# Optimization experiments

Measured on AMD Instinct MI355X. Metric: run time of the kernel, lower is better.

The kernel has to match this reference:

```python
import jax, jax.numpy as jnp
import numpy as np

D_MODEL = 1024
N_HEADS = 16
D_HEAD = D_MODEL // N_HEADS
B = 2
Q_LEN = 1024
MEM_LEN = 1024
K_LEN = MEM_LEN + Q_LEN


def _split_heads(x, n_heads):
    b, t, d = x.shape
    return x.reshape(b, t, n_heads, d // n_heads).transpose(0, 2, 1, 3)


def _rel_shift(x):
    # x: [b, h, q, k] -> Transformer-XL relative shift
    b, h, q_len, k_len = x.shape
    x = jnp.pad(x, ((0, 0), (0, 0), (0, 0), (1, 0)))
    x = x.reshape(b, h, k_len + 1, q_len)
    x = x[:, :, 1:, :]
    return x.reshape(b, h, q_len, k_len)


def setup_inputs() -> dict:
    key = jax.random.key(0)
    ks = jax.random.split(key, 10)
    s = 1.0 / np.sqrt(D_MODEL)  # lecun_normal-ish scale for kernels
    return {
        "h": jax.random.normal(ks[0], (B, Q_LEN, D_MODEL), jnp.float32),
        "mem": jax.random.normal(ks[1], (B, MEM_LEN, D_MODEL), jnp.float32),
        "r": jax.random.normal(ks[2], (K_LEN, D_MODEL), jnp.float32),
        "Wq": jax.random.normal(ks[3], (D_MODEL, D_MODEL), jnp.float32) * s,
        "Wk": jax.random.normal(ks[4], (D_MODEL, D_MODEL), jnp.float32) * s,
        "Wv": jax.random.normal(ks[5], (D_MODEL, D_MODEL), jnp.float32) * s,
        "Wr": jax.random.normal(ks[6], (D_MODEL, D_MODEL), jnp.float32) * s,
        "Wo": jax.random.normal(ks[7], (D_MODEL, D_MODEL), jnp.float32) * s,
        "r_w_bias": jnp.zeros((N_HEADS, D_HEAD), jnp.float32),
        "r_r_bias": jnp.zeros((N_HEADS, D_HEAD), jnp.float32),
    }


def reference(h, mem, r, Wq, Wk, Wv, Wr, Wo, r_w_bias, r_r_bias):
    k_len = mem.shape[1] + h.shape[1]
    cat = jnp.concatenate([mem, h], axis=1)           # [b, k, d]
    q = _split_heads(h @ Wq, N_HEADS)                  # [b, h, q, dh]
    k = _split_heads(cat @ Wk, N_HEADS)                # [b, h, k, dh]
    v = _split_heads(cat @ Wv, N_HEADS)                # [b, h, k, dh]
    r_head = (r @ Wr).reshape(k_len, N_HEADS, D_HEAD).transpose(1, 0, 2)  # [h, k, dh]

    qw = q + r_w_bias[None, :, None, :]
    ac = jnp.einsum('bhqd,bhkd->bhqk', qw, k)          # content score
    qr = q + r_r_bias[None, :, None, :]
    bd = _rel_shift(jnp.einsum('bhqd,hkd->bhqk', qr, r_head))  # position score

    attn_score = (ac + bd) / jnp.sqrt(jnp.array(D_HEAD, jnp.float32))
    attn_prob = jax.nn.softmax(attn_score, axis=-1)
    attn_vec = jnp.einsum('bhqk,bhkd->bhqd', attn_prob, v)
    b, nh, t, dh = attn_vec.shape
    attn_vec = attn_vec.transpose(0, 2, 1, 3).reshape(b, t, nh * dh)
    return attn_vec @ Wo
```

## Files before the change

kernel.cpp:

```cpp
#include <hip/hip_runtime.h>

#define DM 1024
#define NH 16
#define DH 64
#define QL 1024
#define KL 2048

typedef short s16x8 __attribute__((ext_vector_type(8)));
typedef float f32x4 __attribute__((ext_vector_type(4)));

__device__ __forceinline__ unsigned short f2bf(float f) {
  unsigned int u = __builtin_bit_cast(unsigned int, f);
  u += 0x7fffu + ((u >> 16) & 1u);
  return (unsigned short)(u >> 16);
}
__device__ __forceinline__ float bf2f(unsigned short b) {
  unsigned int u = ((unsigned int)b) << 16;
  return __builtin_bit_cast(float, u);
}
__device__ __forceinline__ f32x4 mfma16(s16x8 a, s16x8 b, f32x4 c) {
  return __builtin_amdgcn_mfma_f32_16x16x32_bf16(a, b, c, 0, 0, 0);
}
__device__ __forceinline__ void gl2lds16(const void* g, void* l) {
  __builtin_amdgcn_global_load_lds(
      (const __attribute__((address_space(1))) unsigned int*)g,
      (__attribute__((address_space(3))) unsigned int*)l, 16, 0, 0);
}


__global__ __launch_bounds__(256) void prep_all(
    const float* __restrict__ h, const float* __restrict__ mem, const float* __restrict__ r,
    const float* __restrict__ Wq, const float* __restrict__ Wk, const float* __restrict__ Wv,
    const float* __restrict__ Wr, const float* __restrict__ Wo,
    unsigned short* __restrict__ catb, unsigned short* __restrict__ rb,
    unsigned short* __restrict__ wqt, unsigned short* __restrict__ wkvt,
    unsigned short* __restrict__ wrt,
    unsigned short* __restrict__ wohi, unsigned short* __restrict__ wolo)
{
  __shared__ unsigned short tH[64][72];
  __shared__ unsigned short tL[64][72];
  if (blockIdx.x < 6144) {
    int idx = blockIdx.x * 256 + threadIdx.x;
    if (idx < 1048576) {
      int e = idx * 4;
      int row = e >> 10, col = e & 1023;
      int b = row >> 11, t = row & 2047;
      const float* s = (t < 1024) ? &mem[((size_t)(b * 1024 + t)) * 1024 + col]
                                  : &h[((size_t)(b * 1024 + t - 1024)) * 1024 + col];
      float4 v = *(const float4*)s;
      *(ushort4*)&catb[e] = make_ushort4(f2bf(v.x), f2bf(v.y), f2bf(v.z), f2bf(v.w));
    } else {
      int e = (idx - 1048576) * 4;
      float4 v = *(const float4*)&r[e];
      *(ushort4*)&rb[e] = make_ushort4(f2bf(v.x), f2bf(v.y), f2bf(v.z), f2bf(v.w));
    }
    return;
  }
  int q = blockIdx.x - 6144;
  int job = q >> 8;
  int tb = q & 255;
  int sr0 = (tb >> 4) * 64, sc0 = (tb & 15) * 64;
  const float* src = (job == 0) ? Wq : (job == 1) ? Wk : (job == 2) ? Wv : (job == 3) ? Wr : Wo;
  int tid = threadIdx.x;
  int rr = tid >> 4, c4 = (tid & 15) * 4;
#pragma unroll
  for (int i = 0; i < 4; ++i) {
    int row = rr + i * 16;
    float4 v = *(const float4*)&src[(size_t)(sr0 + row) * 1024 + sc0 + c4];
    float vv[4] = {v.x, v.y, v.z, v.w};
#pragma unroll
    for (int j = 0; j < 4; ++j) {
      unsigned short hi = f2bf(vv[j]);
      tH[c4 + j][row] = hi;
      if (job == 4) tL[c4 + j][row] = f2bf(vv[j] - bf2f(hi));
    }
  }
  __syncthreads();
  unsigned short* dst = (job == 0) ? wqt : (job == 1) ? wkvt
                      : (job == 2) ? (wkvt + (size_t)1024 * 1024)
                      : (job == 3) ? wrt : wohi;
#pragma unroll
  for (int i = 0; i < 4; ++i) {
    int row = rr + i * 16;
    size_t o = (size_t)(sc0 + row) * 1024 + sr0 + c4;
    *(ushort4*)&dst[o] = make_ushort4(tH[row][c4], tH[row][c4 + 1], tH[row][c4 + 2], tH[row][c4 + 3]);
    if (job == 4)
      *(ushort4*)&wolo[o] = make_ushort4(tL[row][c4], tL[row][c4 + 1], tL[row][c4 + 2], tL[row][c4 + 3]);
  }
}

__global__ __launch_bounds__(256) void gemm_all(
    const unsigned short* __restrict__ catb, const unsigned short* __restrict__ rb,
    const unsigned short* __restrict__ wqt, const unsigned short* __restrict__ wkvt,
    const unsigned short* __restrict__ wrt,
    const float* __restrict__ rwb, const float* __restrict__ rrb,
    unsigned short* __restrict__ qwP, unsigned short* __restrict__ qrP,
    unsigned short* __restrict__ kP, unsigned short* __restrict__ vP,
    unsigned short* __restrict__ rP)
{
  __shared__ __align__(16) unsigned short As[2][128 * 32];
  __shared__ __align__(16) unsigned short Bs[2][128 * 32];
  int blk = blockIdx.x, tid = threadIdx.x;
  int job, mb, nb;
  const unsigned short *A, *Bt;
  if (blk < 128)      { job = 0; A = catb; Bt = wqt;  mb = blk >> 3; nb = blk & 7; }
  else if (blk < 640) { job = 1; A = catb; Bt = wkvt; int q = blk - 128; mb = q >> 4; nb = q & 15; }
  else                { job = 2; A = rb;   Bt = wrt;  int q = blk - 640; mb = q >> 3; nb = q & 7; }

  const int w = tid >> 6;
  const int r0 = tid >> 2;
  const int c0u = (tid & 3) * 8;
  int ga_r0 = mb * 128 + r0, ga_r1 = mb * 128 + 64 + r0;
  if (job == 0) {
    ga_r0 = ((ga_r0 >> 10) << 11) + 1024 + (ga_r0 & 1023);
    ga_r1 = ((ga_r1 >> 10) << 11) + 1024 + (ga_r1 & 1023);
  }
  const unsigned short* gA0 = A + (size_t)ga_r0 * 1024 + c0u;
  const unsigned short* gA1 = A + (size_t)ga_r1 * 1024 + c0u;
  const unsigned short* gB0 = Bt + (size_t)(nb * 128 + r0) * 1024 + c0u;
  const unsigned short* gB1 = Bt + (size_t)(nb * 128 + 64 + r0) * 1024 + c0u;

  const int lane = tid & 63;
  const int lc = lane & 15, quad = lane >> 4;
  const int wm = (w & 1) * 64, wn = (w >> 1) * 64;

  auto stage = [&](int k0, int bi) {
    gl2lds16(gA0 + k0, (char*)As[bi] + w * 1024);
    gl2lds16(gA1 + k0, (char*)As[bi] + 4096 + w * 1024);
    gl2lds16(gB0 + k0, (char*)Bs[bi] + w * 1024);
    gl2lds16(gB1 + k0, (char*)Bs[bi] + 4096 + w * 1024);
  };

  f32x4 acc[4][4];
#pragma unroll
  for (int mt = 0; mt < 4; ++mt)
#pragma unroll
    for (int nt = 0; nt < 4; ++nt) { acc[mt][nt][0] = 0.f; acc[mt][nt][1] = 0.f; acc[mt][nt][2] = 0.f; acc[mt][nt][3] = 0.f; }

  stage(0, 0);
  __syncthreads();
  for (int k0 = 0; k0 < 1024; k0 += 32) {
    int cur = (k0 >> 5) & 1;
    if (k0 + 32 < 1024) stage(k0 + 32, cur ^ 1);
    s16x8 af[4], bfr[4];
#pragma unroll
    for (int mt = 0; mt < 4; ++mt) af[mt] = *(const s16x8*)&As[cur][(wm + mt * 16 + lc) * 32 + quad * 8];
#pragma unroll
    for (int nt = 0; nt < 4; ++nt) bfr[nt] = *(const s16x8*)&Bs[cur][(wn + nt * 16 + lc) * 32 + quad * 8];
#pragma unroll
    for (int mt = 0; mt < 4; ++mt)
#pragma unroll
      for (int nt = 0; nt < 4; ++nt) acc[mt][nt] = mfma16(af[mt], bfr[nt], acc[mt][nt]);
    __syncthreads();
  }

#pragma unroll
  for (int mt = 0; mt < 4; ++mt) {
    int t4 = mb * 128 + wm + mt * 16 + quad * 4;
#pragma unroll
    for (int nt = 0; nt < 4; ++nt) {
      int n = nb * 128 + wn + nt * 16 + lc;
      if (job == 0) {
        int hh = n >> 6, dh = n & 63;
        int f = dh >> 5, qd = (dh >> 3) & 3, j = dh & 7;
        float bw = rwb[n], br = rrb[n];
        int bb = t4 >> 10, trow = t4 & 1023;
        size_t tbb = ((((size_t)(bb * NH + hh) * 64 + (trow >> 4)) * 2 + f) * 512) + qd * 128 + j;
        int l0 = trow & 15;
#pragma unroll
        for (int rr = 0; rr < 4; ++rr) {
          qwP[tbb + (l0 + rr) * 8] = f2bf(acc[mt][nt][rr] + bw);
          qrP[tbb + (l0 + rr) * 8] = f2bf(acc[mt][nt][rr] + br);
        }
      } else if (job == 1) {
        int bb = t4 >> 11, t = t4 & 2047;
        if (n < 1024) {
          int hh = n >> 6, dh = n & 63;
          int f = dh >> 5, qd = (dh >> 3) & 3, j = dh & 7;
          size_t tbb = ((((size_t)(bb * NH + hh) * 128 + (t >> 4)) * 2 + f) * 512) + qd * 128 + j;
          int l0 = t & 15;
#pragma unroll
          for (int rr = 0; rr < 4; ++rr)
            kP[tbb + (l0 + rr) * 8] = f2bf(acc[mt][nt][rr]);
        } else {
          int n2 = n - 1024, hh = n2 >> 6, dh = n2 & 63;
          int bhv = bb * NH + hh;
          int kt = t >> 5;
          int ntv = dh >> 4;
          int lanev = (((t >> 3) & 3) << 4) + (dh & 15);
          ushort4 pk = make_ushort4(f2bf(acc[mt][nt][0]), f2bf(acc[mt][nt][1]),
                                    f2bf(acc[mt][nt][2]), f2bf(acc[mt][nt][3]));
          *(ushort4*)&vP[(((size_t)bhv * 64 + kt) * 4 + ntv) * 512 + lanev * 8 + (t & 7)] = pk;
        }
      } else {
        int hh = n >> 6, dh = n & 63;
        int f = dh >> 5, qd = (dh >> 3) & 3, j = dh & 7;
        size_t tbb = (((size_t)hh * 128 + (t4 >> 4)) * 2 + f) * 512 + qd * 128 + j;
        int l0 = t4 & 15;
#pragma unroll
        for (int rr = 0; rr < 4; ++rr)
          rP[tbb + (l0 + rr) * 8] = f2bf(acc[mt][nt][rr]);
      }
    }
  }
}

#define BDSTR 2058
__global__ __launch_bounds__(512, 4) void attn(
    const unsigned short* __restrict__ qwP, const unsigned short* __restrict__ qrP,
    const unsigned short* __restrict__ kP, const unsigned short* __restrict__ vP,
    const unsigned short* __restrict__ rP,
    unsigned short* __restrict__ avhi, unsigned short* __restrict__ avlo)
{
  __shared__ __align__(16) unsigned short bdS[17 * BDSTR];
  __shared__ __align__(16) unsigned short pS[8 * 16 * 36];
  float* oS = (float*)bdS;
  float* lS = (float*)bdS + 8192;

  const int tid = threadIdx.x;
  const int w = tid >> 6, lane = tid & 63;
  const int lc = lane & 15, quad = lane >> 4;
  const int is = blockIdx.x & 63, h = (blockIdx.x >> 6) & 15, b = blockIdx.x >> 10;
  const int i0 = is * 16;
  const size_t bh = (size_t)b * NH + h;

  const unsigned short* qwP_p = qwP + bh * 65536;
  const unsigned short* qrP_p = qrP + bh * 65536;
  const unsigned short* kP_p  = kP + bh * 131072;
  const unsigned short* vP_p  = vP + bh * (size_t)KL * DH + lane * 8;
  const unsigned short* rP_p  = rP + (size_t)h * 131072;

  {
    const int cmax = 1006 - i0;
    s16x8 qa00 = *(const s16x8*)(qrP_p + is * 1024 + lane * 8);
    s16x8 qa01 = *(const s16x8*)(qrP_p + is * 1024 + 512 + lane * 8);
    int r1 = i0 + 16 + lc; if (r1 > 1023) r1 = 1023;
    int off1 = (r1 >> 4) * 1024 + (quad * 16 + (r1 & 15)) * 8;
    s16x8 qa10 = *(const s16x8*)(qrP_p + off1);
    s16x8 qa11 = *(const s16x8*)(qrP_p + off1 + 512);
    const int xt0 = w * 16;
    const unsigned short* rp = rP_p + xt0 * 1024 + lane * 8;
    s16x8 rf0 = *(const s16x8*)rp;
    s16x8 rf1 = *(const s16x8*)(rp + 512);
    for (int xt = xt0; xt < xt0 + 16; ++xt) {
      s16x8 cf0 = rf0, cf1 = rf1;
      if (xt + 1 < xt0 + 16) {
        const unsigned short* rpn = rP_p + (xt + 1) * 1024 + lane * 8;
        rf0 = *(const s16x8*)rpn;
        rf1 = *(const s16x8*)(rpn + 512);
      }
      f32x4 c0; c0[0] = 0.f; c0[1] = 0.f; c0[2] = 0.f; c0[3] = 0.f;
      c0 = mfma16(qa00, cf0, c0); c0 = mfma16(qa01, cf1, c0);
      int col = xt * 16 + lc;
#pragma unroll
      for (int rr = 0; rr < 4; ++rr) bdS[(quad * 4 + rr) * BDSTR + col] = f2bf(c0[rr]);
      if (xt * 16 <= cmax) {
        f32x4 c1; c1[0] = 0.f; c1[1] = 0.f; c1[2] = 0.f; c1[3] = 0.f;
        c1 = mfma16(qa10, cf0, c1); c1 = mfma16(qa11, cf1, c1);
        if (lane < 16) bdS[16 * BDSTR + col] = f2bf(c1[0]);
      }
    }
  }
  __syncthreads();

  s16x8 qwf0 = *(const s16x8*)(qwP_p + is * 1024 + lane * 8);
  s16x8 qwf1 = *(const s16x8*)(qwP_p + is * 1024 + 512 + lane * 8);

  f32x4 O[4];
#pragma unroll
  for (int nt = 0; nt < 4; ++nt) { O[nt][0] = 0.f; O[nt][1] = 0.f; O[nt][2] = 0.f; O[nt][3] = 0.f; }
  float lsum[4] = {0.f, 0.f, 0.f, 0.f};
  unsigned short* pw = pS + w * 16 * 36;
  int ebase[4];
#pragma unroll
  for (int rr = 0; rr < 4; ++rr) ebase[rr] = lc - (quad * 4 + rr) - i0;

  auto gatherBD = [&](int k0, float bd[2][4]) {
#pragma unroll
    for (int tt = 0; tt < 2; ++tt)
#pragma unroll
      for (int rr = 0; rr < 4; ++rr) {
        int row = quad * 4 + rr;
        int d = k0 + tt * 16 + ebase[rr];
        int am = row * BDSTR + (d + 1023);
        int aw = (row + 1) * BDSTR + (d - 1026);
        unsigned short vb = bdS[(d <= 1024) ? am : aw];
        bd[tt][rr] = (d == 1025) ? 0.0f : bf2f(vb);
      }
  };
  auto loadK4 = [&](int k0, s16x8& a0, s16x8& a1, s16x8& b0, s16x8& b1) {
    const unsigned short* kp = kP_p + (size_t)(k0 >> 4) * 1024 + lane * 8;
    a0 = *(const s16x8*)kp;
    a1 = *(const s16x8*)(kp + 512);
    b0 = *(const s16x8*)(kp + 1024);
    b1 = *(const s16x8*)(kp + 1536);
  };
  const float E2S = 0.18033688011112042f;
  const float E2B = -17.312340490667562f;
  auto qkExp = [&](const s16x8& a0, const s16x8& a1, const s16x8& b0, const s16x8& b1,
                   const float bd[2][4], float p[2][4]) {
    f32x4 c;
    c[0] = bd[0][0]; c[1] = bd[0][1]; c[2] = bd[0][2]; c[3] = bd[0][3];
    c = mfma16(qwf0, a0, c);
    c = mfma16(qwf1, a1, c);
#pragma unroll
    for (int rr = 0; rr < 4; ++rr) {
      p[0][rr] = __builtin_amdgcn_exp2f(fmaf(c[rr], E2S, E2B));
      lsum[rr] += p[0][rr];
    }
    f32x4 d;
    d[0] = bd[1][0]; d[1] = bd[1][1]; d[2] = bd[1][2]; d[3] = bd[1][3];
    d = mfma16(qwf0, b0, d);
    d = mfma16(qwf1, b1, d);
#pragma unroll
    for (int rr = 0; rr < 4; ++rr) {
      p[1][rr] = __builtin_amdgcn_exp2f(fmaf(d[rr], E2S, E2B));
      lsum[rr] += p[1][rr];
    }
  };
  auto storeP = [&](float p[2][4]) {
#pragma unroll
    for (int rr = 0; rr < 4; ++rr) {
      int row = quad * 4 + rr;
      pw[row * 36 + lc]      = f2bf(p[0][rr]);
      pw[row * 36 + 16 + lc] = f2bf(p[1][rr]);
    }
  };
  auto loadV = [&](int k0, s16x8 vf[4]) {
    const unsigned short* base = vP_p + (size_t)(k0 >> 5) * 2048;
#pragma unroll
    for (int nt = 0; nt < 4; ++nt)
      vf[nt] = *(const s16x8*)(base + nt * 512);
  };

  const int base = w * 256;
  s16x8 ka0, ka1, kb0, kb1;
  s16x8 vf[4];
  s16x8 pf;
  float bd[2][4], nbd[2][4];

  gatherBD(base, bd);
  loadK4(base, ka0, ka1, kb0, kb1);
  loadV(base, vf);
  {
    float p[2][4];
    gatherBD(base + 32, nbd);
    s16x8 na0, na1, nb0, nb1;
    loadK4(base + 32, na0, na1, nb0, nb1);
    qkExp(ka0, ka1, kb0, kb1, bd, p);
    storeP(p);
    pf = *(const s16x8*)(pw + lc * 36 + quad * 8);
    ka0 = na0; ka1 = na1; kb0 = nb0; kb1 = nb1;
#pragma unroll
    for (int tt = 0; tt < 2; ++tt)
#pragma unroll
      for (int rr = 0; rr < 4; ++rr) bd[tt][rr] = nbd[tt][rr];
  }
#pragma unroll 1
  for (int s = 1; s < 8; ++s) {
    const int k0 = base + s * 32;
    const int kn = base + ((s < 7) ? (s + 1) * 32 : s * 32);
    float p[2][4];
    gatherBD(kn, nbd);
    s16x8 na0, na1, nb0, nb1;
    loadK4(kn, na0, na1, nb0, nb1);
    qkExp(ka0, ka1, kb0, kb1, bd, p);
#pragma unroll
    for (int nt = 0; nt < 4; ++nt) O[nt] = mfma16(pf, vf[nt], O[nt]);
    loadV(k0, vf);
    storeP(p);
    pf = *(const s16x8*)(pw + lc * 36 + quad * 8);
    ka0 = na0; ka1 = na1; kb0 = nb0; kb1 = nb1;
#pragma unroll
    for (int tt = 0; tt < 2; ++tt)
#pragma unroll
      for (int rr = 0; rr < 4; ++rr) bd[tt][rr] = nbd[tt][rr];
  }
  {
#pragma unroll
    for (int nt = 0; nt < 4; ++nt) O[nt] = mfma16(pf, vf[nt], O[nt]);
  }

#pragma unroll
  for (int msk = 1; msk <= 8; msk <<= 1)
#pragma unroll
    for (int rr = 0; rr < 4; ++rr) lsum[rr] += __shfl_xor(lsum[rr], msk);

  __syncthreads();
#pragma unroll
  for (int nt = 0; nt < 4; ++nt)
#pragma unroll
    for (int rr = 0; rr < 4; ++rr)
      oS[(w * 16 + quad * 4 + rr) * 64 + nt * 16 + lc] = O[nt][rr];
  if (lc == 0) {
#pragma unroll
    for (int rr = 0; rr < 4; ++rr) lS[w * 16 + quad * 4 + rr] = lsum[rr];
  }
  __syncthreads();

  if (tid < 256) {
    int r = tid >> 4, c0 = (tid & 15) * 4;
    float L = 0.f, a0 = 0.f, a1 = 0.f, a2 = 0.f, a3 = 0.f;
#pragma unroll
    for (int wv = 0; wv < 8; ++wv) {
      L += lS[wv * 16 + r];
      const float* op = oS + (wv * 16 + r) * 64 + c0;
      a0 += op[0]; a1 += op[1]; a2 += op[2]; a3 += op[3];
    }
    float inv = 1.0f / L;
    float v[4] = {a0 * inv, a1 * inv, a2 * inv, a3 * inv};
    unsigned short hi[4], lo[4];
#pragma unroll
    for (int j = 0; j < 4; ++j) {
      hi[j] = f2bf(v[j]);
      lo[j] = f2bf(v[j] - bf2f(hi[j]));
    }
    size_t oidx = ((size_t)(b * QL + i0 + r)) * DM + h * DH + c0;
    *(ushort4*)&avhi[oidx] = make_ushort4(hi[0], hi[1], hi[2], hi[3]);
    *(ushort4*)&avlo[oidx] = make_ushort4(lo[0], lo[1], lo[2], lo[3]);
  }
}

__global__ __launch_bounds__(256) void gemm_final(
    const unsigned short* __restrict__ avhi, const unsigned short* __restrict__ avlo,
    const unsigned short* __restrict__ wohi, const unsigned short* __restrict__ wolo,
    float* __restrict__ out)
{
  __shared__ __align__(16) unsigned short S[2][4][64 * 32];
  int blk = blockIdx.x, tid = threadIdx.x;
  int mb = blk >> 4, nb = blk & 15;

  const int w = tid >> 6, lane = tid & 63;
  const int srow = w * 16 + (lane >> 2);
  const int scu = (lane & 3) * 8;
  const size_t arow = (size_t)(mb * 64 + srow) * 1024 + scu;
  const size_t brow = (size_t)(nb * 64 + srow) * 1024 + scu;

  const int lc = lane & 15, quad = lane >> 4;
  const int wm = (w & 1) * 32, wn = (w >> 1) * 32;

  auto stage = [&](int k0, int bi) {
    gl2lds16(avhi + arow + k0, (char*)S[bi][0] + w * 1024);
    gl2lds16(avlo + arow + k0, (char*)S[bi][1] + w * 1024);
    gl2lds16(wohi + brow + k0, (char*)S[bi][2] + w * 1024);
    gl2lds16(wolo + brow + k0, (char*)S[bi][3] + w * 1024);
  };

  f32x4 acc[2][2];
#pragma unroll
  for (int mt = 0; mt < 2; ++mt)
#pragma unroll
    for (int nt = 0; nt < 2; ++nt) { acc[mt][nt][0] = 0.f; acc[mt][nt][1] = 0.f; acc[mt][nt][2] = 0.f; acc[mt][nt][3] = 0.f; }

  stage(0, 0);
  __syncthreads();
  for (int k0 = 0; k0 < 1024; k0 += 32) {
    int cur = (k0 >> 5) & 1;
    if (k0 + 32 < 1024) stage(k0 + 32, cur ^ 1);
    s16x8 ah[2], al[2], bh[2], bl[2];
#pragma unroll
    for (int mt = 0; mt < 2; ++mt) {
      int off = (wm + mt * 16 + lc) * 32 + quad * 8;
      ah[mt] = *(const s16x8*)&S[cur][0][off];
      al[mt] = *(const s16x8*)&S[cur][1][off];
    }
#pragma unroll
    for (int nt = 0; nt < 2; ++nt) {
      int off = (wn + nt * 16 + lc) * 32 + quad * 8;
      bh[nt] = *(const s16x8*)&S[cur][2][off];
      bl[nt] = *(const s16x8*)&S[cur][3][off];
    }
#pragma unroll
    for (int mt = 0; mt < 2; ++mt)
#pragma unroll
      for (int nt = 0; nt < 2; ++nt) {
        acc[mt][nt] = mfma16(ah[mt], bh[nt], acc[mt][nt]);
        acc[mt][nt] = mfma16(ah[mt], bl[nt], acc[mt][nt]);
        acc[mt][nt] = mfma16(al[mt], bh[nt], acc[mt][nt]);
      }
    __syncthreads();
  }

#pragma unroll
  for (int mt = 0; mt < 2; ++mt)
#pragma unroll
    for (int nt = 0; nt < 2; ++nt) {
      int n = nb * 64 + wn + nt * 16 + lc;
#pragma unroll
      for (int rr = 0; rr < 4; ++rr) {
        int m = mb * 64 + wm + mt * 16 + quad * 4 + rr;
        out[(size_t)m * 1024 + n] = acc[mt][nt][rr];
      }
    }
}

extern "C" void kernel_launch(void* const* d_in, const int* in_sizes, int n_in,
                              void* d_out, int out_size, void* d_ws, size_t ws_size,
                              hipStream_t stream) {
  (void)in_sizes; (void)n_in; (void)out_size; (void)ws_size;
  const float* h   = (const float*)d_in[0];
  const float* mem = (const float*)d_in[1];
  const float* r   = (const float*)d_in[2];
  const float* Wq  = (const float*)d_in[3];
  const float* Wk  = (const float*)d_in[4];
  const float* Wv  = (const float*)d_in[5];
  const float* Wr  = (const float*)d_in[6];
  const float* Wo  = (const float*)d_in[7];
  const float* rwb = (const float*)d_in[8];
  const float* rrb = (const float*)d_in[9];
  float* out = (float*)d_out;

  char* ws = (char*)d_ws;
  unsigned short* catb = (unsigned short*)(ws + 0);
  unsigned short* rb   = (unsigned short*)(ws + 8388608);
  unsigned short* wqt  = (unsigned short*)(ws + 12582912);
  unsigned short* wkvt = (unsigned short*)(ws + 14680064);
  unsigned short* wrt  = (unsigned short*)(ws + 18874368);
  unsigned short* wohi = (unsigned short*)(ws + 20971520);
  unsigned short* wolo = (unsigned short*)(ws + 23068672);
  unsigned short* qwP  = (unsigned short*)(ws + 25165824);
  unsigned short* qrP  = (unsigned short*)(ws + 29360128);
  unsigned short* kPb  = (unsigned short*)(ws + 33554432);
  unsigned short* vPb  = (unsigned short*)(ws + 41943040);
  unsigned short* rPb  = (unsigned short*)(ws + 50331648);
  unsigned short* avhi = (unsigned short*)(ws + 54525952);
  unsigned short* avlo = (unsigned short*)(ws + 58720256);

  prep_all<<<7424, 256, 0, stream>>>(h, mem, r, Wq, Wk, Wv, Wr, Wo,
                                     catb, rb, wqt, wkvt, wrt, wohi, wolo);
  gemm_all<<<768, 256, 0, stream>>>(catb, rb, wqt, wkvt, wrt, rwb, rrb,
                                    qwP, qrP, kPb, vPb, rPb);
  attn<<<2048, 512, 0, stream>>>(qwP, qrP, kPb, vPb, rPb, avhi, avlo);
  gemm_final<<<512, 256, 0, stream>>>(avhi, avlo, wohi, wolo, out);
}
```

Baseline: 239.9 us.

## Transpose attention MFMAs to keep P in registers and pre-shift BD in LDS

The attention loop swaps the MFMA operand order so the score tile comes out key-major. The exp'd probabilities then pack straight into the B operand of the PV MFMA through v_cvt_pk_bf16_f32, with no LDS round-trip for P. The relative-shift position scores are written into LDS already shifted, so the main loop reads them with one vectorized load instead of per-element gathers with branches. The V packing layout is changed to match the new operand order, blocks are remapped across XCDs, and the output staging stride is padded against bank conflicts. This removes LDS traffic and ALU work from the inner loop, but the shift, zeroing and layout index math must all be exactly right.

```diff
diff --git a/kernel.cpp b/kernel.cpp
--- a/kernel.cpp
+++ b/kernel.cpp
@@ -8,6 +8,7 @@
 
 typedef short s16x8 __attribute__((ext_vector_type(8)));
 typedef float f32x4 __attribute__((ext_vector_type(4)));
+typedef unsigned int u32x4 __attribute__((ext_vector_type(4)));
 
 __device__ __forceinline__ unsigned short f2bf(float f) {
   unsigned int u = __builtin_bit_cast(unsigned int, f);
@@ -187,10 +188,11 @@
           int bhv = bb * NH + hh;
           int kt = t >> 5;
           int ntv = dh >> 4;
-          int lanev = (((t >> 3) & 3) << 4) + (dh & 15);
+          int lanev = (((t >> 2) & 3) << 4) + (dh & 15);
+          int elemv = ((t >> 4) & 1) << 2;
           ushort4 pk = make_ushort4(f2bf(acc[mt][nt][0]), f2bf(acc[mt][nt][1]),
                                     f2bf(acc[mt][nt][2]), f2bf(acc[mt][nt][3]));
-          *(ushort4*)&vP[(((size_t)bhv * 64 + kt) * 4 + ntv) * 512 + lanev * 8 + (t & 7)] = pk;
+          *(ushort4*)&vP[(((size_t)bhv * 64 + kt) * 4 + ntv) * 512 + lanev * 8 + elemv] = pk;
         }
       } else {
         int hh = n >> 6, dh = n & 63;
@@ -205,22 +207,23 @@
   }
 }
 
-#define BDSTR 2058
+#define BDSTR 2060
+#define OSTR 65
 __global__ __launch_bounds__(512, 4) void attn(
     const unsigned short* __restrict__ qwP, const unsigned short* __restrict__ qrP,
     const unsigned short* __restrict__ kP, const unsigned short* __restrict__ vP,
     const unsigned short* __restrict__ rP,
     unsigned short* __restrict__ avhi, unsigned short* __restrict__ avlo)
 {
-  __shared__ __align__(16) unsigned short bdS[17 * BDSTR];
-  __shared__ __align__(16) unsigned short pS[8 * 16 * 36];
+  __shared__ __align__(16) unsigned short bdS[16 * BDSTR];
   float* oS = (float*)bdS;
-  float* lS = (float*)bdS + 8192;
+  float* lS = (float*)bdS + 8 * 16 * OSTR;
 
   const int tid = threadIdx.x;
   const int w = tid >> 6, lane = tid & 63;
   const int lc = lane & 15, quad = lane >> 4;
-  const int is = blockIdx.x & 63, h = (blockIdx.x >> 6) & 15, b = blockIdx.x >> 10;
+  const int sem = (blockIdx.x & 7) * 256 + (blockIdx.x >> 3);
+  const int is = sem & 63, h = (sem >> 6) & 15, b = sem >> 10;
   const int i0 = is * 16;
   const size_t bh = (size_t)b * NH + h;
 
@@ -229,6 +232,11 @@
   const unsigned short* kP_p  = kP + bh * 131072;
   const unsigned short* vP_p  = vP + bh * (size_t)KL * DH + lane * 8;
   const unsigned short* rP_p  = rP + (size_t)h * 131072;
+
+  if (tid < 16) {
+    int kz = i0 + tid + 1025;
+    if (kz < 2048) bdS[tid * BDSTR + kz] = 0;
+  }
 
   {
     const int cmax = 1006 - i0;
@@ -242,6 +250,7 @@
     const unsigned short* rp = rP_p + xt0 * 1024 + lane * 8;
     s16x8 rf0 = *(const s16x8*)rp;
     s16x8 rf1 = *(const s16x8*)(rp + 512);
+    const int rbq = quad * 4 * BDSTR;
     for (int xt = xt0; xt < xt0 + 16; ++xt) {
       s16x8 cf0 = rf0, cf1 = rf1;
       if (xt + 1 < xt0 + 16) {
@@ -251,13 +260,22 @@
       }
       f32x4 c0; c0[0] = 0.f; c0[1] = 0.f; c0[2] = 0.f; c0[3] = 0.f;
       c0 = mfma16(qa00, cf0, c0); c0 = mfma16(qa01, cf1, c0);
-      int col = xt * 16 + lc;
-#pragma unroll
-      for (int rr = 0; rr < 4; ++rr) bdS[(quad * 4 + rr) * BDSTR + col] = f2bf(c0[rr]);
+      int c = xt * 16 + lc;
+#pragma unroll
+      for (int rr = 0; rr < 4; ++rr) {
+        int row = quad * 4 + rr;
+        int s = c + i0 + row - 1023;
+        int off = (s < 0) ? (s - 12) : s;
+        if (!(row == 0 && s < 0))
+          bdS[rbq + rr * BDSTR + off] = f2bf(c0[rr]);
+      }
       if (xt * 16 <= cmax) {
         f32x4 c1; c1[0] = 0.f; c1[1] = 0.f; c1[2] = 0.f; c1[3] = 0.f;
         c1 = mfma16(qa10, cf0, c1); c1 = mfma16(qa11, cf1, c1);
-        if (lane < 16) bdS[16 * BDSTR + col] = f2bf(c1[0]);
+        if (lane < 16) {
+          int key2 = c + i0 + 1041;
+          if (key2 < 2048) bdS[15 * BDSTR + key2] = f2bf(c1[0]);
+        }
       }
     }
   }
@@ -269,25 +287,13 @@
   f32x4 O[4];
 #pragma unroll
   for (int nt = 0; nt < 4; ++nt) { O[nt][0] = 0.f; O[nt][1] = 0.f; O[nt][2] = 0.f; O[nt][3] = 0.f; }
-  float lsum[4] = {0.f, 0.f, 0.f, 0.f};
-  unsigned short* pw = pS + w * 16 * 36;
-  int ebase[4];
-#pragma unroll
-  for (int rr = 0; rr < 4; ++rr) ebase[rr] = lc - (quad * 4 + rr) - i0;
-
-  auto gatherBD = [&](int k0, float bd[2][4]) {
-#pragma unroll
-    for (int tt = 0; tt < 2; ++tt)
-#pragma unroll
-      for (int rr = 0; rr < 4; ++rr) {
-        int row = quad * 4 + rr;
-        int d = k0 + tt * 16 + ebase[rr];
-        int am = row * BDSTR + (d + 1023);
-        int aw = (row + 1) * BDSTR + (d - 1026);
-        unsigned short vb = bdS[(d <= 1024) ? am : aw];
-        bd[tt][rr] = (d == 1025) ? 0.0f : bf2f(vb);
-      }
-  };
+  float lsumQ = 0.f;
+
+  const unsigned short* bdlane = bdS + lc * BDSTR + quad * 4;
+  const int base = w * 256;
+  const float E2S = 0.18033688011112042f;
+  const float E2B = -17.312340490667562f;
+
   auto loadK4 = [&](int k0, s16x8& a0, s16x8& a1, s16x8& b0, s16x8& b1) {
     const unsigned short* kp = kP_p + (size_t)(k0 >> 4) * 1024 + lane * 8;
     a0 = *(const s16x8*)kp;
@@ -295,107 +301,80 @@
     b0 = *(const s16x8*)(kp + 1024);
     b1 = *(const s16x8*)(kp + 1536);
   };
-  const float E2S = 0.18033688011112042f;
-  const float E2B = -17.312340490667562f;
-  auto qkExp = [&](const s16x8& a0, const s16x8& a1, const s16x8& b0, const s16x8& b1,
-                   const float bd[2][4], float p[2][4]) {
+  auto loadV4 = [&](int k0, s16x8& x0, s16x8& x1, s16x8& x2, s16x8& x3) {
+    const unsigned short* bp = vP_p + (size_t)(k0 >> 5) * 2048;
+    x0 = *(const s16x8*)bp;
+    x1 = *(const s16x8*)(bp + 512);
+    x2 = *(const s16x8*)(bp + 1024);
+    x3 = *(const s16x8*)(bp + 1536);
+  };
+
+  s16x8 ka0, ka1, kb0, kb1, v0, v1, v2, v3;
+  uint2 bq0 = *(const uint2*)(bdlane + base);
+  uint2 bq1 = *(const uint2*)(bdlane + base + 16);
+  loadK4(base, ka0, ka1, kb0, kb1);
+  loadV4(base, v0, v1, v2, v3);
+
+#pragma unroll 1
+  for (int s = 0; s < 8; ++s) {
+    const int k0 = base + s * 32;
+    const int kn = (s < 7) ? (k0 + 32) : k0;
+    uint2 nq0 = *(const uint2*)(bdlane + kn);
+    uint2 nq1 = *(const uint2*)(bdlane + kn + 16);
+    s16x8 na0, na1, nb0, nb1;  loadK4(kn, na0, na1, nb0, nb1);
+    s16x8 nv0, nv1, nv2, nv3;  loadV4(kn, nv0, nv1, nv2, nv3);
+
     f32x4 c;
-    c[0] = bd[0][0]; c[1] = bd[0][1]; c[2] = bd[0][2]; c[3] = bd[0][3];
-    c = mfma16(qwf0, a0, c);
-    c = mfma16(qwf1, a1, c);
+    c[0] = __builtin_bit_cast(float, bq0.x << 16);
+    c[1] = __builtin_bit_cast(float, bq0.x & 0xFFFF0000u);
+    c[2] = __builtin_bit_cast(float, bq0.y << 16);
+    c[3] = __builtin_bit_cast(float, bq0.y & 0xFFFF0000u);
+    c = mfma16(ka0, qwf0, c);
+    c = mfma16(ka1, qwf1, c);
+    f32x4 d;
+    d[0] = __builtin_bit_cast(float, bq1.x << 16);
+    d[1] = __builtin_bit_cast(float, bq1.x & 0xFFFF0000u);
+    d[2] = __builtin_bit_cast(float, bq1.y << 16);
+    d[3] = __builtin_bit_cast(float, bq1.y & 0xFFFF0000u);
+    d = mfma16(kb0, qwf0, d);
+    d = mfma16(kb1, qwf1, d);
+
+    float p0[4], p1[4];
 #pragma unroll
     for (int rr = 0; rr < 4; ++rr) {
-      p[0][rr] = __builtin_amdgcn_exp2f(fmaf(c[rr], E2S, E2B));
-      lsum[rr] += p[0][rr];
-    }
-    f32x4 d;
-    d[0] = bd[1][0]; d[1] = bd[1][1]; d[2] = bd[1][2]; d[3] = bd[1][3];
-    d = mfma16(qwf0, b0, d);
-    d = mfma16(qwf1, b1, d);
-#pragma unroll
-    for (int rr = 0; rr < 4; ++rr) {
-      p[1][rr] = __builtin_amdgcn_exp2f(fmaf(d[rr], E2S, E2B));
-      lsum[rr] += p[1][rr];
-    }
-  };
-  auto storeP = [&](float p[2][4]) {
-#pragma unroll
-    for (int rr = 0; rr < 4; ++rr) {
-      int row = quad * 4 + rr;
-      pw[row * 36 + lc]      = f2bf(p[0][rr]);
-      pw[row * 36 + 16 + lc] = f2bf(p[1][rr]);
-    }
-  };
-  auto loadV = [&](int k0, s16x8 vf[4]) {
-    const unsigned short* base = vP_p + (size_t)(k0 >> 5) * 2048;
-#pragma unroll
-    for (int nt = 0; nt < 4; ++nt)
-      vf[nt] = *(const s16x8*)(base + nt * 512);
-  };
-
-  const int base = w * 256;
-  s16x8 ka0, ka1, kb0, kb1;
-  s16x8 vf[4];
-  s16x8 pf;
-  float bd[2][4], nbd[2][4];
-
-  gatherBD(base, bd);
-  loadK4(base, ka0, ka1, kb0, kb1);
-  loadV(base, vf);
-  {
-    float p[2][4];
-    gatherBD(base + 32, nbd);
-    s16x8 na0, na1, nb0, nb1;
-    loadK4(base + 32, na0, na1, nb0, nb1);
-    qkExp(ka0, ka1, kb0, kb1, bd, p);
-    storeP(p);
-    pf = *(const s16x8*)(pw + lc * 36 + quad * 8);
+      p0[rr] = __builtin_amdgcn_exp2f(fmaf(c[rr], E2S, E2B));
+      p1[rr] = __builtin_amdgcn_exp2f(fmaf(d[rr], E2S, E2B));
+    }
+    lsumQ += ((p0[0] + p0[1]) + (p0[2] + p0[3])) + ((p1[0] + p1[1]) + (p1[2] + p1[3]));
+
+    unsigned int w0, w1, w2, w3;
+    asm("v_cvt_pk_bf16_f32 %0, %1, %2" : "=v"(w0) : "v"(p0[0]), "v"(p0[1]));
+    asm("v_cvt_pk_bf16_f32 %0, %1, %2" : "=v"(w1) : "v"(p0[2]), "v"(p0[3]));
+    asm("v_cvt_pk_bf16_f32 %0, %1, %2" : "=v"(w2) : "v"(p1[0]), "v"(p1[1]));
+    asm("v_cvt_pk_bf16_f32 %0, %1, %2" : "=v"(w3) : "v"(p1[2]), "v"(p1[3]));
+    u32x4 pw4 = {w0, w1, w2, w3};
+    s16x8 pf = __builtin_bit_cast(s16x8, pw4);
+
+    O[0] = mfma16(v0, pf, O[0]);
+    O[1] = mfma16(v1, pf, O[1]);
+    O[2] = mfma16(v2, pf, O[2]);
+    O[3] = mfma16(v3, pf, O[3]);
+
+    bq0 = nq0; bq1 = nq1;
     ka0 = na0; ka1 = na1; kb0 = nb0; kb1 = nb1;
-#pragma unroll
-    for (int tt = 0; tt < 2; ++tt)
-#pragma unroll
-      for (int rr = 0; rr < 4; ++rr) bd[tt][rr] = nbd[tt][rr];
-  }
-#pragma unroll 1
-  for (int s = 1; s < 8; ++s) {
-    const int k0 = base + s * 32;
-    const int kn = base + ((s < 7) ? (s + 1) * 32 : s * 32);
-    float p[2][4];
-    gatherBD(kn, nbd);
-    s16x8 na0, na1, nb0, nb1;
-    loadK4(kn, na0, na1, nb0, nb1);
-    qkExp(ka0, ka1, kb0, kb1, bd, p);
-#pragma unroll
-    for (int nt = 0; nt < 4; ++nt) O[nt] = mfma16(pf, vf[nt], O[nt]);
-    loadV(k0, vf);
-    storeP(p);
-    pf = *(const s16x8*)(pw + lc * 36 + quad * 8);
-    ka0 = na0; ka1 = na1; kb0 = nb0; kb1 = nb1;
-#pragma unroll
-    for (int tt = 0; tt < 2; ++tt)
-#pragma unroll
-      for (int rr = 0; rr < 4; ++rr) bd[tt][rr] = nbd[tt][rr];
-  }
-  {
-#pragma unroll
-    for (int nt = 0; nt < 4; ++nt) O[nt] = mfma16(pf, vf[nt], O[nt]);
-  }
-
-#pragma unroll
-  for (int msk = 1; msk <= 8; msk <<= 1)
-#pragma unroll
-    for (int rr = 0; rr < 4; ++rr) lsum[rr] += __shfl_xor(lsum[rr], msk);
+    v0 = nv0; v1 = nv1; v2 = nv2; v3 = nv3;
+  }
+
+  lsumQ += __shfl_xor(lsumQ, 16);
+  lsumQ += __shfl_xor(lsumQ, 32);
 
   __syncthreads();
 #pragma unroll
   for (int nt = 0; nt < 4; ++nt)
 #pragma unroll
     for (int rr = 0; rr < 4; ++rr)
-      oS[(w * 16 + quad * 4 + rr) * 64 + nt * 16 + lc] = O[nt][rr];
-  if (lc == 0) {
-#pragma unroll
-    for (int rr = 0; rr < 4; ++rr) lS[w * 16 + quad * 4 + rr] = lsum[rr];
-  }
+      oS[(w * 16 + lc) * OSTR + nt * 16 + quad * 4 + rr] = O[nt][rr];
+  if (lane < 16) lS[w * 16 + lc] = lsumQ;
   __syncthreads();
 
   if (tid < 256) {
@@ -404,7 +383,7 @@
 #pragma unroll
     for (int wv = 0; wv < 8; ++wv) {
       L += lS[wv * 16 + r];
-      const float* op = oS + (wv * 16 + r) * 64 + c0;
+      const float* op = oS + (wv * 16 + r) * OSTR + c0;
       a0 += op[0]; a1 += op[1]; a2 += op[2]; a3 += op[3];
     }
     float inv = 1.0f / L;
```

New measurement: 226.5 us. 5.6% less time.
